# Optimization experiments

Measured on AMD Instinct MI355X. Metric: run time of the kernel, lower is better.

Reference implementation:

```python
import jax, jax.numpy as jnp
import numpy as np

CHUNK = 1024  # rows of the query cloud processed per tile; avoids NxM materialization


def _nn_sq_dist(a, b):
    """Per-point squared distance from each row of a (N,3) to its nearest row of b (M,3).

    Chunked over a so the live intermediate is (CHUNK, M), mirroring the tiled
    chamfer3D CUDA kernel instead of a full cdist.
    """
    b_sq = jnp.sum(b * b, axis=1)  # (M,)

    def tile_min(ac):  # ac: (CHUNK, 3)
        # squared euclidean: |a|^2 + |b|^2 - 2 a.b
        d = jnp.sum(ac * ac, axis=1)[:, None] + b_sq[None, :] - 2.0 * (ac @ b.T)
        return jnp.min(d, axis=1)  # (CHUNK,)

    n = a.shape[0]
    a_tiles = a.reshape(n // CHUNK, CHUNK, 3)
    mins = jax.lax.map(tile_min, a_tiles)  # (n//CHUNK, CHUNK)
    return mins.reshape(n)


def setup_inputs() -> dict:
    key = jax.random.key(0)
    k0, k1 = jax.random.split(key)
    N, M = 65536, 65536
    pc0 = jax.random.normal(k0, (N, 3), dtype=jnp.float32) * 10.0
    pc1 = jax.random.normal(k1, (M, 3), dtype=jnp.float32) * 10.0
    return {"pc0": pc0, "pc1": pc1}


def reference(pc0, pc1):
    # nnChamferDis.forward with truncate_dist <= 0 (default):
    # mean of squared NN distance in both directions.
    d0 = _nn_sq_dist(pc0, pc1)  # (N,) dist of each pc0 point to nearest pc1 point
    d1 = _nn_sq_dist(pc1, pc0)  # (M,)
    return jnp.mean(d0) + jnp.mean(d1)
```

## Files before the change

kernel.cpp:

```cpp
#include <hip/hip_runtime.h>

typedef unsigned int u32;

#define NPTS 65536
#define G    24
#define NC   (G*G*G)
#define CPT  14

#define CNTA_OFF 0u
#define CNTB_OFF (CNTA_OFF + NC*4u)
#define HDRA_OFF (CNTB_OFF + NC*4u)
#define HDRB_OFF (HDRA_OFF + NC*8u)
#define SRTA_OFF (HDRB_OFF + NC*8u)
#define SRTB_OFF (SRTA_OFF + NPTS*16u)

__device__ __forceinline__ int clampi(int v, int lo, int hi) {
    return v < lo ? lo : (v > hi ? hi : v);
}

__device__ __forceinline__ int cell1(float x) {
    const float kk = 0.07071067811865475f;
    return clampi((int)(0.5f * erfcf(-x * kk) * (float)G), 0, G - 1);
}
__device__ __forceinline__ void cell3(float x, float y, float z,
                                      int& cx, int& cy, int& cz) {
    cx = cell1(x); cy = cell1(y); cz = cell1(z);
}

__global__ __launch_bounds__(256) void count_kernel(
    const float* __restrict__ A, const float* __restrict__ B,
    unsigned char* __restrict__ ws)
{
    const int i = blockIdx.x * 256 + threadIdx.x;
    const int cloud = i >= NPTS;
    const int p = i & (NPTS - 1);
    const float* __restrict__ P = cloud ? B : A;
    u32* cnt = (u32*)(ws + (cloud ? CNTB_OFF : CNTA_OFF));
    int cx, cy, cz;
    cell3(P[p * 3], P[p * 3 + 1], P[p * 3 + 2], cx, cy, cz);
    atomicAdd(&cnt[(cz * G + cy) * G + cx], 1u);
}

__global__ __launch_bounds__(1024) void scan_kernel(unsigned char* __restrict__ ws)
{
    const int cloud = blockIdx.x;
    const u32* cnt = (const u32*)(ws + (cloud ? CNTB_OFF : CNTA_OFF));
    uint2* hdr = (uint2*)(ws + (cloud ? HDRB_OFF : HDRA_OFF));
    const int t = threadIdx.x;

    u32 s = 0;
#pragma unroll
    for (int k = 0; k < CPT; ++k) {
        const int c = t * CPT + k;
        s += (c < NC) ? cnt[c] : 0u;
    }
    __shared__ u32 lds[1024];
    lds[t] = s;
    __syncthreads();
    for (int o = 1; o < 1024; o <<= 1) {
        const u32 v = (t >= o) ? lds[t - o] : 0u;
        __syncthreads();
        lds[t] += v;
        __syncthreads();
    }
    u32 run = lds[t] - s;
#pragma unroll
    for (int k = 0; k < CPT; ++k) {
        const int c = t * CPT + k;
        if (c < NC) {
            const u32 n = cnt[c];
            hdr[c] = make_uint2(run, n);
            run += n;
        }
    }
}

__global__ __launch_bounds__(256) void scatter_kernel(
    const float* __restrict__ A, const float* __restrict__ B,
    unsigned char* __restrict__ ws)
{
    const int i = blockIdx.x * 256 + threadIdx.x;
    const int cloud = i >= NPTS;
    const int p = i & (NPTS - 1);
    const float* __restrict__ P = cloud ? B : A;
    u32* cnt = (u32*)(ws + (cloud ? CNTB_OFF : CNTA_OFF));
    const uint2* hdr = (const uint2*)(ws + (cloud ? HDRB_OFF : HDRA_OFF));
    float4* srt = (float4*)(ws + (cloud ? SRTB_OFF : SRTA_OFF));

    const float x = P[p * 3], y = P[p * 3 + 1], z = P[p * 3 + 2];
    int cx, cy, cz;
    cell3(x, y, z, cx, cy, cz);
    const int c = (cz * G + cy) * G + cx;
    const u32 old = atomicSub(&cnt[c], 1u);
    srt[hdr[c].x + old - 1u] = make_float4(x, y, z, 0.0f);
}

__global__ __launch_bounds__(256) void query_kernel(
    const unsigned char* __restrict__ ws, float* __restrict__ out)
{
    const int wv   = blockIdx.x * 4 + (threadIdx.x >> 6);
    const int lane = threadIdx.x & 63;
    const int dirB = wv >= NC;
    const int c    = dirB ? wv - NC : wv;
    const int cx = c % G, cy = (c / G) % G, cz = c / (G * G);

    const uint2*  __restrict__ qhdr = (const uint2*)(ws + (dirB ? HDRB_OFF : HDRA_OFF));
    const float4* __restrict__ qp   = (const float4*)(ws + (dirB ? SRTB_OFF : SRTA_OFF));
    const uint2*  __restrict__ dhdr = (const uint2*)(ws + (dirB ? HDRA_OFF : HDRB_OFF));
    const float4* __restrict__ dbp  = (const float4*)(ws + (dirB ? SRTA_OFF : SRTB_OFF));

    const uint2 qh = qhdr[c];
    float qsum = 0.0f;

    if (qh.y != 0) {
        const int x0 = max(cx - 1, 0), x1 = min(cx + 1, G - 1);
        const int rowb = (cz * G + cy) * G;
        const uint2 h0 = dhdr[rowb + x0];
        const uint2 h1 = dhdr[rowb + x1];
        const u32 s0 = h0.x, s1 = h1.x + h1.y;

        for (u32 j = 0; j < qh.y; ++j) {
            const float4 q = qp[qh.x + j];
            float best = 3.4e38f;

            for (u32 k = s0 + lane; k < s1; k += 64) {
                const float4 p = dbp[k];
                const float dx = q.x - p.x, dy = q.y - p.y, dz = q.z - p.z;
                best = fminf(best, fmaf(dx, dx, fmaf(dy, dy, dz * dz)));
            }
#pragma unroll
            for (int m = 1; m <= 32; m <<= 1)
                best = fminf(best, __shfl_xor(best, m, 64));

            const float rad = sqrtf(best) + 1e-3f;
            const int lox = cell1(q.x - rad), hix = cell1(q.x + rad);
            const int loy = cell1(q.y - rad), hiy = cell1(q.y + rad);
            const int loz = cell1(q.z - rad), hiz = cell1(q.z + rad);

            const bool skip = (lox >= x0) && (hix <= x1) &&
                              (loy == cy) && (hiy == cy) &&
                              (loz == cz) && (hiz == cz);
            if (!skip) {
                const int ny = hiy - loy + 1;
                const int R  = ny * (hiz - loz + 1);
                for (int rb = 0; rb < R; rb += 64) {
                    const int r = rb + lane;
                    if (r < R) {
                        const int yy = loy + r % ny;
                        const int zz = loz + r / ny;
                        const int base = (zz * G + yy) * G;
                        const uint2 ha = dhdr[base + lox];
                        const uint2 hb = dhdr[base + hix];
                        for (u32 k = ha.x; k < hb.x + hb.y; ++k) {
                            const float4 p = dbp[k];
                            const float dx = q.x - p.x, dy = q.y - p.y, dz = q.z - p.z;
                            best = fminf(best, fmaf(dx, dx, fmaf(dy, dy, dz * dz)));
                        }
                    }
                }
#pragma unroll
                for (int m = 1; m <= 32; m <<= 1)
                    best = fminf(best, __shfl_xor(best, m, 64));
            }
            if (lane == 0) qsum += best;
        }
    }

    __shared__ float wsum[4];
    if (lane == 0) wsum[threadIdx.x >> 6] = qsum;
    __syncthreads();
    if (threadIdx.x == 0)
        atomicAdd(out, (wsum[0] + wsum[1] + wsum[2] + wsum[3]) * (1.0f / (float)NPTS));
}

extern "C" void kernel_launch(void* const* d_in, const int* in_sizes, int n_in,
                              void* d_out, int out_size, void* d_ws, size_t ws_size,
                              hipStream_t stream)
{
    const float* A = (const float*)d_in[0];
    const float* B = (const float*)d_in[1];
    float* out = (float*)d_out;
    unsigned char* ws = (unsigned char*)d_ws;

    hipMemsetAsync(ws + CNTA_OFF, 0, 2u * NC * 4u, stream);
    hipMemsetAsync(out, 0, sizeof(float), stream);

    count_kernel  <<<(2 * NPTS) / 256, 256, 0, stream>>>(A, B, ws);
    scan_kernel   <<<2, 1024, 0, stream>>>(ws);
    scatter_kernel<<<(2 * NPTS) / 256, 256, 0, stream>>>(A, B, ws);
    query_kernel  <<<(2 * NC) / 4, 256, 0, stream>>>(ws, out);
}
```

Baseline: 199.2 us.

## Process two queries per wavefront and replace erfc cell lookup with LDS boundary table

Each 64-lane wavefront now splits into two 32-lane halves, each handling its own query point, so cells with few candidate points keep more lanes busy. The per-query erfc-based cell computation for the search box is replaced by a linear walk over a shared-memory table of cell boundaries built with erfinv at block start. Each query's box is padded by a small epsilon to stay conservative. The trade-offs are narrower per-query parallelism, an added block-level sync, per-block table setup, and divergent while loops.

```diff
diff --git a/kernel.cpp b/kernel.cpp
--- a/kernel.cpp
+++ b/kernel.cpp
@@ -98,8 +98,21 @@
 __global__ __launch_bounds__(256) void query_kernel(
     const unsigned char* __restrict__ ws, float* __restrict__ out)
 {
+    __shared__ float XB[G + 1];
+    if (threadIdx.x <= G) {
+        float v;
+        if (threadIdx.x == 0)       v = -3e37f;
+        else if (threadIdx.x == G)  v =  3e37f;
+        else v = 14.142135623730951f *
+                 erfinvf(2.0f * (float)threadIdx.x / (float)G - 1.0f);
+        XB[threadIdx.x] = v;
+    }
+    __syncthreads();
+
     const int wv   = blockIdx.x * 4 + (threadIdx.x >> 6);
     const int lane = threadIdx.x & 63;
+    const int half = lane >> 5;
+    const int sub  = lane & 31;
     const int dirB = wv >= NC;
     const int c    = dirB ? wv - NC : wv;
     const int cx = c % G, cy = (c / G) % G, cz = c / (G * G);
@@ -119,23 +132,31 @@
         const uint2 h1 = dhdr[rowb + x1];
         const u32 s0 = h0.x, s1 = h1.x + h1.y;
 
-        for (u32 j = 0; j < qh.y; ++j) {
-            const float4 q = qp[qh.x + j];
+        for (u32 j = 0; j < qh.y; j += 2) {
+            const u32  jj  = j + (u32)half;
+            const bool act = jj < qh.y;
+            const float4 q = qp[qh.x + (act ? jj : 0u)];
             float best = 3.4e38f;
 
-            for (u32 k = s0 + lane; k < s1; k += 64) {
+            for (u32 k = s0 + sub; k < s1; k += 32) {
                 const float4 p = dbp[k];
                 const float dx = q.x - p.x, dy = q.y - p.y, dz = q.z - p.z;
                 best = fminf(best, fmaf(dx, dx, fmaf(dy, dy, dz * dz)));
             }
 #pragma unroll
-            for (int m = 1; m <= 32; m <<= 1)
+            for (int m = 1; m <= 16; m <<= 1)
                 best = fminf(best, __shfl_xor(best, m, 64));
 
             const float rad = sqrtf(best) + 1e-3f;
-            const int lox = cell1(q.x - rad), hix = cell1(q.x + rad);
-            const int loy = cell1(q.y - rad), hiy = cell1(q.y + rad);
-            const int loz = cell1(q.z - rad), hiz = cell1(q.z + rad);
+            const float qxl = q.x - rad - 1e-3f, qxh = q.x + rad + 1e-3f;
+            const float qyl = q.y - rad - 1e-3f, qyh = q.y + rad + 1e-3f;
+            const float qzl = q.z - rad - 1e-3f, qzh = q.z + rad + 1e-3f;
+            int lox = cx; while (lox > 0     && XB[lox]     > qxl) --lox;
+            int hix = cx; while (hix < G - 1 && XB[hix + 1] < qxh) ++hix;
+            int loy = cy; while (loy > 0     && XB[loy]     > qyl) --loy;
+            int hiy = cy; while (hiy < G - 1 && XB[hiy + 1] < qyh) ++hiy;
+            int loz = cz; while (loz > 0     && XB[loz]     > qzl) --loz;
+            int hiz = cz; while (hiz < G - 1 && XB[hiz + 1] < qzh) ++hiz;
 
             const bool skip = (lox >= x0) && (hix <= x1) &&
                               (loy == cy) && (hiy == cy) &&
@@ -143,15 +164,16 @@
             if (!skip) {
                 const int ny = hiy - loy + 1;
                 const int R  = ny * (hiz - loz + 1);
-                for (int rb = 0; rb < R; rb += 64) {
-                    const int r = rb + lane;
+                for (int rb = 0; rb < R; rb += 32) {
+                    const int r = rb + sub;
                     if (r < R) {
                         const int yy = loy + r % ny;
                         const int zz = loz + r / ny;
                         const int base = (zz * G + yy) * G;
                         const uint2 ha = dhdr[base + lox];
                         const uint2 hb = dhdr[base + hix];
-                        for (u32 k = ha.x; k < hb.x + hb.y; ++k) {
+                        const u32 e = hb.x + hb.y;
+                        for (u32 k = ha.x; k < e; ++k) {
                             const float4 p = dbp[k];
                             const float dx = q.x - p.x, dy = q.y - p.y, dz = q.z - p.z;
                             best = fminf(best, fmaf(dx, dx, fmaf(dy, dy, dz * dz)));
@@ -159,10 +181,15 @@
                     }
                 }
 #pragma unroll
-                for (int m = 1; m <= 32; m <<= 1)
+                for (int m = 1; m <= 16; m <<= 1)
                     best = fminf(best, __shfl_xor(best, m, 64));
             }
-            if (lane == 0) qsum += best;
+
+            const float b1 = __shfl(best, 32, 64);
+            if (lane == 0) {
+                qsum += best;
+                if (j + 1 < qh.y) qsum += b1;
+            }
         }
     }
 
```

Result: faster. 174.7 us (-12.3%).
